# Kernel optimization log

Hardware: AMD Instinct MI355X
Metric: run time of the kernel (lower is better)

Reference implementation:

```python
import jax, jax.numpy as jnp
import numpy as np

_EPS = 1e-8

def setup_inputs() -> dict:
    key = jax.random.key(0)
    k1, k2, k3, k4 = jax.random.split(key, 4)
    L, B, H, S = 12, 8, 12, 384
    M, NL, NH = 32, 3, 4
    attn = jax.random.uniform(k1, (L, B, H, S, S), dtype=jnp.float32)
    references = jax.random.uniform(k2, (M, S, S), dtype=jnp.float32)
    layer_idx = jax.random.randint(k3, (M, NL), 0, L)
    head_idx = jax.random.randint(k4, (M, NH), 0, H)
    return {"attn": attn, "references": references,
            "layer_idx": layer_idx, "head_idx": head_idx}

def reference(attn, references, layer_idx, head_idx):
    # attn: [L,B,H,S,S] stacked attention maps; references: [M,S,S]
    L, B, H, S, _ = attn.shape
    M, nl = layer_idx.shape
    nh = head_idx.shape[1]
    rows = jnp.arange(M)[:, None]
    # One-hot averaging matrices: patch mean over selected layers/heads.
    # .add handles repeated indices the same way the gather-then-mean does.
    Wl = jnp.zeros((M, L), attn.dtype).at[rows, layer_idx].add(1.0 / nl)
    Wh = jnp.zeros((M, H), attn.dtype).at[rows, head_idx].add(1.0 / nh)
    # patch_means[m,b,s,t] = mean over patch layers/heads of attn
    patch_means = jnp.einsum('ml,mh,lbhst->mbst', Wl, Wh, attn)  # [M,B,S,S]
    flat = patch_means.reshape(M, B, S * S)
    ref = references.reshape(M, 1, S * S)
    # torch .std is unbiased (ddof=1) over the batch axis
    std = jnp.maximum(jnp.std(flat, axis=1, ddof=1, keepdims=True), _EPS)
    z = (flat - ref) / std
    scores = jnp.mean(z * z, axis=-1)  # [M,B]
    return scores.T  # [B,M]
```

## Files before the change

kernel.cpp:

```cpp
#include <hip/hip_runtime.h>

#define L_DIM 12
#define B_DIM 8
#define H_DIM 12
#define S2    147456
#define M_DIM 32
#define NL 3
#define NH 4
#define HS2   (H_DIM * S2)

#define C      128
#define NCH    (S2 / C)
#define RED1   32
#define NRED1  (NCH / RED1)

#define PART_FLOATS (NCH * 256)
#define MID_FLOATS  (NRED1 * 256)
#define META_INTS   2048

__global__ __launch_bounds__(256) void pfe_setup(
    const int* __restrict__ lidx, const int* __restrict__ hidx, int* __restrict__ mi)
{
    __shared__ unsigned char s_cl[M_DIM][16];
    __shared__ unsigned char s_ch[M_DIM][16];
    __shared__ int s_used[144];
    __shared__ int s_slot[144];
    const int t = threadIdx.x;
    for (int i = t; i < 1176; i += 256) mi[168 + i] = 0;
    if (t < M_DIM) {
        for (int l = 0; l < L_DIM; ++l) s_cl[t][l] = 0;
        for (int h = 0; h < H_DIM; ++h) s_ch[t][h] = 0;
        for (int i = 0; i < NL; ++i) s_cl[t][lidx[t * NL + i]]++;
        for (int j = 0; j < NH; ++j) s_ch[t][hidx[t * NH + j]]++;
    }
    __syncthreads();
    if (t < 144) {
        const int l = t / H_DIM, h = t % H_DIM;
        int u = 0;
        for (int m = 0; m < M_DIM; ++m) u |= (s_cl[m][l] && s_ch[m][h]) ? 1 : 0;
        s_used[t] = u;
    }
    __syncthreads();
    if (t == 0) {
        int np = 0, lastb = 0;
        for (int k = 0; k < 144; ++k) {
            if (s_used[k]) {
                s_slot[k] = np;
                lastb = ((k / H_DIM) * (B_DIM * H_DIM) + (k % H_DIM)) * S2;
                mi[8 + np] = lastb;
                ++np;
            } else s_slot[k] = -1;
        }
        for (int p = np; p < 160; ++p) mi[8 + p] = lastb;
        mi[0] = np;
    }
    __syncthreads();
    if (t < 144) {
        const int sl = s_slot[t];
        if (sl >= 0) {
            const int l = t / H_DIM, h = t % H_DIM;
            int wd[8] = {0, 0, 0, 0, 0, 0, 0, 0};
#pragma unroll
            for (int g = 0; g < 8; ++g) {
                int w = 0;
#pragma unroll
                for (int j = 0; j < 4; ++j) {
                    const int m = g * 4 + j;
                    w |= ((int)s_cl[m][l] * (int)s_ch[m][h]) << (8 * j);
                }
                wd[g] = w;
            }
            int* wp = mi + 168 + sl * 8;
#pragma unroll
            for (int g = 0; g < 8; ++g) wp[g] = wd[g];
        }
    }
}

__global__ __launch_bounds__(256) void pfe_gather(
    const float* __restrict__ attn, const float* __restrict__ refs,
    const int* __restrict__ mi, float* __restrict__ part)
{
    __shared__ int s_pbase[160];
    __shared__ int s_ww[1176];
    __shared__ float s_x[8 * B_DIM * C];

    const int t = threadIdx.x;
    for (int i = t; i < 160; i += 256) s_pbase[i] = mi[8 + i];
    for (int i = t; i < 1176; i += 256) s_ww[i] = mi[168 + i];
    const int np4 = (mi[0] + 3) & ~3;
    __syncthreads();

    const int b = t >> 5, q = t & 31;
    const unsigned off0 = (unsigned)blockIdx.x * C;
    const unsigned fixoff = (unsigned)b * (unsigned)HS2 + off0 + (unsigned)q * 4u;

    float4 acc[M_DIM];
#pragma unroll
    for (int m = 0; m < M_DIM; ++m) acc[m] = make_float4(0.f, 0.f, 0.f, 0.f);

#define LD(P) (*reinterpret_cast<const float4*>(attn + (unsigned)s_pbase[P] + fixoff))

#define PROC_WORD(SW, G, V)                                             \
    if (SW) {                                                           \
        const float f0 = (float)((SW) & 255);                           \
        const float f1 = (float)(((SW) >> 8) & 255);                    \
        const float f2 = (float)(((SW) >> 16) & 255);                   \
        const float f3 = (float)(((SW) >> 24) & 255);                   \
        acc[4*(G)+0].x = fmaf(f0, (V).x, acc[4*(G)+0].x);               \
        acc[4*(G)+0].y = fmaf(f0, (V).y, acc[4*(G)+0].y);               \
        acc[4*(G)+0].z = fmaf(f0, (V).z, acc[4*(G)+0].z);               \
        acc[4*(G)+0].w = fmaf(f0, (V).w, acc[4*(G)+0].w);               \
        acc[4*(G)+1].x = fmaf(f1, (V).x, acc[4*(G)+1].x);               \
        acc[4*(G)+1].y = fmaf(f1, (V).y, acc[4*(G)+1].y);               \
        acc[4*(G)+1].z = fmaf(f1, (V).z, acc[4*(G)+1].z);               \
        acc[4*(G)+1].w = fmaf(f1, (V).w, acc[4*(G)+1].w);               \
        acc[4*(G)+2].x = fmaf(f2, (V).x, acc[4*(G)+2].x);               \
        acc[4*(G)+2].y = fmaf(f2, (V).y, acc[4*(G)+2].y);               \
        acc[4*(G)+2].z = fmaf(f2, (V).z, acc[4*(G)+2].z);               \
        acc[4*(G)+2].w = fmaf(f2, (V).w, acc[4*(G)+2].w);               \
        acc[4*(G)+3].x = fmaf(f3, (V).x, acc[4*(G)+3].x);               \
        acc[4*(G)+3].y = fmaf(f3, (V).y, acc[4*(G)+3].y);               \
        acc[4*(G)+3].z = fmaf(f3, (V).z, acc[4*(G)+3].z);               \
        acc[4*(G)+3].w = fmaf(f3, (V).w, acc[4*(G)+3].w);               \
    }

#define PROC_PLANE(P, V)                                                \
    {                                                                   \
        const int4 wa = *reinterpret_cast<const int4*>(s_ww + (P) * 8); \
        const int4 wb = *reinterpret_cast<const int4*>(s_ww + (P) * 8 + 4); \
        const int w0 = __builtin_amdgcn_readfirstlane(wa.x);            \
        const int w1 = __builtin_amdgcn_readfirstlane(wa.y);            \
        const int w2 = __builtin_amdgcn_readfirstlane(wa.z);            \
        const int w3 = __builtin_amdgcn_readfirstlane(wa.w);            \
        const int w4 = __builtin_amdgcn_readfirstlane(wb.x);            \
        const int w5 = __builtin_amdgcn_readfirstlane(wb.y);            \
        const int w6 = __builtin_amdgcn_readfirstlane(wb.z);            \
        const int w7 = __builtin_amdgcn_readfirstlane(wb.w);            \
        PROC_WORD(w0, 0, V) PROC_WORD(w1, 1, V)                         \
        PROC_WORD(w2, 2, V) PROC_WORD(w3, 3, V)                         \
        PROC_WORD(w4, 4, V) PROC_WORD(w5, 5, V)                         \
        PROC_WORD(w6, 6, V) PROC_WORD(w7, 7, V)                         \
    }

    float4 n0 = LD(0), n1 = LD(1), n2 = LD(2), n3 = LD(3);
    for (int p = 0; p < np4; p += 4) {
        const float4 c0 = n0, c1 = n1, c2 = n2, c3 = n3;
        n0 = LD(p + 4); n1 = LD(p + 5); n2 = LD(p + 6); n3 = LD(p + 7);
        PROC_PLANE(p + 0, c0)
        PROC_PLANE(p + 1, c1)
        PROC_PLANE(p + 2, c2)
        PROC_PLANE(p + 3, c3)
    }
#undef PROC_PLANE
#undef PROC_WORD
#undef LD

    const float c12 = 1.0f / 12.0f;
    const int mm = t >> 5;

    for (int sl = 0; sl < 4; ++sl) {
        __syncthreads();
#pragma unroll
        for (int k = 0; k < 8; ++k) {
            const float4 a = acc[sl * 8 + k];
            float4 p;
            p.x = a.x * c12; p.y = a.y * c12; p.z = a.z * c12; p.w = a.w * c12;
            *reinterpret_cast<float4*>(&s_x[(k * B_DIM + b) * C + q * 4]) = p;
        }
        __syncthreads();

        const int m = sl * 8 + mm;
        float4 x[B_DIM];
#pragma unroll
        for (int bb = 0; bb < B_DIM; ++bb)
            x[bb] = *reinterpret_cast<const float4*>(&s_x[(mm * B_DIM + bb) * C + q * 4]);
        float4 mu = make_float4(0.f, 0.f, 0.f, 0.f);
#pragma unroll
        for (int bb = 0; bb < B_DIM; ++bb) {
            mu.x += x[bb].x; mu.y += x[bb].y; mu.z += x[bb].z; mu.w += x[bb].w;
        }
        mu.x *= 0.125f; mu.y *= 0.125f; mu.z *= 0.125f; mu.w *= 0.125f;
        float4 ss = make_float4(0.f, 0.f, 0.f, 0.f);
#pragma unroll
        for (int bb = 0; bb < B_DIM; ++bb) {
            const float dx = x[bb].x - mu.x, dy = x[bb].y - mu.y,
                        dz = x[bb].z - mu.z, dw = x[bb].w - mu.w;
            ss.x = fmaf(dx, dx, ss.x); ss.y = fmaf(dy, dy, ss.y);
            ss.z = fmaf(dz, dz, ss.z); ss.w = fmaf(dw, dw, ss.w);
        }
        const float c7 = 1.0f / 7.0f;
        float4 inv;
        inv.x = 1.0f / fmaxf(sqrtf(ss.x * c7), 1e-8f);
        inv.y = 1.0f / fmaxf(sqrtf(ss.y * c7), 1e-8f);
        inv.z = 1.0f / fmaxf(sqrtf(ss.z * c7), 1e-8f);
        inv.w = 1.0f / fmaxf(sqrtf(ss.w * c7), 1e-8f);
        const float4 rv = *reinterpret_cast<const float4*>(
            refs + (size_t)m * S2 + off0 + (unsigned)q * 4u);

        float zs[B_DIM];
#pragma unroll
        for (int bb = 0; bb < B_DIM; ++bb) {
            const float zx = (x[bb].x - rv.x) * inv.x;
            const float zy = (x[bb].y - rv.y) * inv.y;
            const float zz = (x[bb].z - rv.z) * inv.z;
            const float zw = (x[bb].w - rv.w) * inv.w;
            zs[bb] = fmaf(zx, zx, fmaf(zy, zy, fmaf(zz, zz, zw * zw)));
        }
#pragma unroll
        for (int bb = 0; bb < B_DIM; ++bb) {
            float v = zs[bb];
            v += __shfl_xor(v, 1);
            v += __shfl_xor(v, 2);
            v += __shfl_xor(v, 4);
            v += __shfl_xor(v, 8);
            v += __shfl_xor(v, 16);
            zs[bb] = v;
        }
        if (q == 0) {
            float* pp = part + blockIdx.x * 256 + m * B_DIM;
            *reinterpret_cast<float4*>(pp) =
                make_float4(zs[0], zs[1], zs[2], zs[3]);
            *reinterpret_cast<float4*>(pp + 4) =
                make_float4(zs[4], zs[5], zs[6], zs[7]);
        }
    }
}

__global__ __launch_bounds__(256) void pfe_red1(
    const float* __restrict__ part, float* __restrict__ mid)
{
    const int t = threadIdx.x;
    const int c0 = blockIdx.x * RED1;
    float s = 0.f;
#pragma unroll
    for (int i = 0; i < RED1; ++i) s += part[(c0 + i) * 256 + t];
    mid[blockIdx.x * 256 + t] = s;
}

__global__ __launch_bounds__(256) void pfe_red2(
    const float* __restrict__ mid, float* __restrict__ out)
{
    const int t = threadIdx.x;
    float s = 0.f;
#pragma unroll
    for (int i = 0; i < NRED1; ++i) s += mid[i * 256 + t];
    out[(t & 7) * M_DIM + (t >> 3)] = s * (1.0f / (float)S2);
}

__global__ void pfe_zero(float* __restrict__ out) {
    if (threadIdx.x < M_DIM * B_DIM) out[threadIdx.x] = 0.f;
}

#define FCH 512
#define FNCH (S2 / FCH)
__global__ __launch_bounds__(128) void pfe_fallback(
    const float* __restrict__ attn, const float* __restrict__ refs,
    const int* __restrict__ lidx, const int* __restrict__ hidx,
    float* __restrict__ out)
{
    const int p = blockIdx.x;
    const int m = p & (M_DIM - 1);
    const int chunk = p >> 5;
    const int tid = threadIdx.x;
    const unsigned st = (unsigned)chunk * FCH + (unsigned)tid * 4;

    __shared__ int   s_mk[NL * NH];
    __shared__ float s_mw[NL * NH];
    __shared__ int   s_nm;
    __shared__ float s_red[2 * B_DIM];

    if (tid == 0) {
        int keys[NL * NH];
        for (int i = 0; i < NL; ++i) {
            const int l = lidx[m * NL + i];
            for (int j = 0; j < NH; ++j) keys[i * NH + j] = l * 16 + hidx[m * NH + j];
        }
        for (int i = 1; i < NL * NH; ++i) {
            const int k = keys[i]; int j = i - 1;
            for (; j >= 0 && keys[j] > k; --j) keys[j + 1] = keys[j];
            keys[j + 1] = k;
        }
        int nm = 0;
        for (int i = 0; i < NL * NH; ++i) {
            if (nm > 0 && s_mk[nm - 1] == keys[i]) s_mw[nm - 1] += 1.0f;
            else { s_mk[nm] = keys[i]; s_mw[nm] = 1.0f; ++nm; }
        }
        s_nm = nm;
    }
    __syncthreads();

    const float4 r = *reinterpret_cast<const float4*>(refs + (unsigned)m * (unsigned)S2 + st);
    float4 acc[B_DIM];
    for (int bb = 0; bb < B_DIM; ++bb) acc[bb] = make_float4(0.f, 0.f, 0.f, 0.f);
    const int nm = s_nm;
    for (int e = 0; e < nm; ++e) {
        const int k = s_mk[e]; const float w = s_mw[e];
        const int l = k >> 4, h = k & 15;
        const unsigned base = (unsigned)(l * (B_DIM * H_DIM) + h) * (unsigned)S2 + st;
        for (int bb = 0; bb < B_DIM; ++bb) {
            const float4 v = *reinterpret_cast<const float4*>(
                attn + base + (unsigned)bb * (unsigned)HS2);
            acc[bb].x = fmaf(w, v.x, acc[bb].x); acc[bb].y = fmaf(w, v.y, acc[bb].y);
            acc[bb].z = fmaf(w, v.z, acc[bb].z); acc[bb].w = fmaf(w, v.w, acc[bb].w);
        }
    }
    const float c12 = 1.0f / 12.0f;
    float4 pmv[B_DIM];
    for (int bb = 0; bb < B_DIM; ++bb) {
        pmv[bb].x = acc[bb].x * c12; pmv[bb].y = acc[bb].y * c12;
        pmv[bb].z = acc[bb].z * c12; pmv[bb].w = acc[bb].w * c12;
    }
    float4 mu = make_float4(0.f, 0.f, 0.f, 0.f);
    for (int bb = 0; bb < B_DIM; ++bb) {
        mu.x += pmv[bb].x; mu.y += pmv[bb].y; mu.z += pmv[bb].z; mu.w += pmv[bb].w;
    }
    mu.x *= 0.125f; mu.y *= 0.125f; mu.z *= 0.125f; mu.w *= 0.125f;
    float4 ss = make_float4(0.f, 0.f, 0.f, 0.f);
    for (int bb = 0; bb < B_DIM; ++bb) {
        const float dx = pmv[bb].x - mu.x, dy = pmv[bb].y - mu.y,
                    dz = pmv[bb].z - mu.z, dw = pmv[bb].w - mu.w;
        ss.x += dx * dx; ss.y += dy * dy; ss.z += dz * dz; ss.w += dw * dw;
    }
    const float c7 = 1.0f / 7.0f;
    float4 inv;
    inv.x = 1.0f / fmaxf(sqrtf(ss.x * c7), 1e-8f);
    inv.y = 1.0f / fmaxf(sqrtf(ss.y * c7), 1e-8f);
    inv.z = 1.0f / fmaxf(sqrtf(ss.z * c7), 1e-8f);
    inv.w = 1.0f / fmaxf(sqrtf(ss.w * c7), 1e-8f);
    float s[B_DIM];
    for (int bb = 0; bb < B_DIM; ++bb) {
        const float zx = (pmv[bb].x - r.x) * inv.x;
        const float zy = (pmv[bb].y - r.y) * inv.y;
        const float zz = (pmv[bb].z - r.z) * inv.z;
        const float zw = (pmv[bb].w - r.w) * inv.w;
        s[bb] = zx * zx + zy * zy + zz * zz + zw * zw;
    }
    for (int bb = 0; bb < B_DIM; ++bb) {
        float v = s[bb];
        for (int off = 32; off > 0; off >>= 1) v += __shfl_down(v, off);
        s[bb] = v;
    }
    const int lane = tid & 63, wave = tid >> 6;
    if (lane == 0) for (int bb = 0; bb < B_DIM; ++bb) s_red[wave * B_DIM + bb] = s[bb];
    __syncthreads();
    if (tid < B_DIM) {
        const float tot = (s_red[tid] + s_red[B_DIM + tid]) * (1.0f / (float)S2);
        atomicAdd(&out[tid * M_DIM + m], tot);
    }
}

extern "C" void kernel_launch(void* const* d_in, const int* in_sizes, int n_in,
                              void* d_out, int out_size, void* d_ws, size_t ws_size,
                              hipStream_t stream) {
    const float* attn = (const float*)d_in[0];
    const float* refs = (const float*)d_in[1];
    const int*   lidx = (const int*)d_in[2];
    const int*   hidx = (const int*)d_in[3];
    float* out = (float*)d_out;

    const size_t ws_needed =
        (size_t)(PART_FLOATS + MID_FLOATS + META_INTS) * sizeof(float);

    if (ws_size >= ws_needed) {
        float* part = (float*)d_ws;
        float* mid  = part + PART_FLOATS;
        int*   mi   = (int*)(mid + MID_FLOATS);
        pfe_setup<<<1, 256, 0, stream>>>(lidx, hidx, mi);
        pfe_gather<<<NCH, 256, 0, stream>>>(attn, refs, mi, part);
        pfe_red1<<<NRED1, 256, 0, stream>>>(part, mid);
        pfe_red2<<<1, 256, 0, stream>>>(mid, out);
    } else {
        pfe_zero<<<1, 256, 0, stream>>>(out);
        pfe_fallback<<<FNCH * M_DIM, 128, 0, stream>>>(attn, refs, lidx, hidx, out);
    }
}
```

Measured before the change: 164.3 us.

## Halve per-thread gather width to float2 with 512-thread blocks for occupancy

The gather kernel now uses 512 threads per block, each handling two columns instead of four. This halves the accumulator registers (32 float2 instead of 32 float4) so more waves can be resident to hide memory latency. It also deepens the load prefetch from 4 to 8 planes and prefetches the reference values one slice ahead. In exchange each load is narrower (8-byte instead of 16-byte), and the cross-lane reduction needs an extra shuffle step because the batch groups are now full 64-lane wavefronts.

```diff
diff --git a/kernel.cpp b/kernel.cpp
--- a/kernel.cpp
+++ b/kernel.cpp
@@ -77,7 +77,7 @@
     }
 }
 
-__global__ __launch_bounds__(256) void pfe_gather(
+__global__ __launch_bounds__(512, 4) void pfe_gather(
     const float* __restrict__ attn, const float* __restrict__ refs,
     const int* __restrict__ mi, float* __restrict__ part)
 {
@@ -86,20 +86,20 @@
     __shared__ float s_x[8 * B_DIM * C];
 
     const int t = threadIdx.x;
-    for (int i = t; i < 160; i += 256) s_pbase[i] = mi[8 + i];
-    for (int i = t; i < 1176; i += 256) s_ww[i] = mi[168 + i];
-    const int np4 = (mi[0] + 3) & ~3;
-    __syncthreads();
-
-    const int b = t >> 5, q = t & 31;
+    for (int i = t; i < 160; i += 512) s_pbase[i] = mi[8 + i];
+    for (int i = t; i < 1176; i += 512) s_ww[i] = mi[168 + i];
+    const int np8 = (mi[0] + 7) & ~7;
+    __syncthreads();
+
+    const int b = t >> 6, q = t & 63;
     const unsigned off0 = (unsigned)blockIdx.x * C;
-    const unsigned fixoff = (unsigned)b * (unsigned)HS2 + off0 + (unsigned)q * 4u;
-
-    float4 acc[M_DIM];
-#pragma unroll
-    for (int m = 0; m < M_DIM; ++m) acc[m] = make_float4(0.f, 0.f, 0.f, 0.f);
-
-#define LD(P) (*reinterpret_cast<const float4*>(attn + (unsigned)s_pbase[P] + fixoff))
+    const unsigned fixoff = (unsigned)b * (unsigned)HS2 + off0 + (unsigned)q * 2u;
+
+    float2 acc[M_DIM];
+#pragma unroll
+    for (int m = 0; m < M_DIM; ++m) acc[m] = make_float2(0.f, 0.f);
+
+#define LD(P) (*reinterpret_cast<const float2*>(attn + (unsigned)s_pbase[P] + fixoff))
 
 #define PROC_WORD(SW, G, V)                                             \
     if (SW) {                                                           \
@@ -109,20 +109,12 @@
         const float f3 = (float)(((SW) >> 24) & 255);                   \
         acc[4*(G)+0].x = fmaf(f0, (V).x, acc[4*(G)+0].x);               \
         acc[4*(G)+0].y = fmaf(f0, (V).y, acc[4*(G)+0].y);               \
-        acc[4*(G)+0].z = fmaf(f0, (V).z, acc[4*(G)+0].z);               \
-        acc[4*(G)+0].w = fmaf(f0, (V).w, acc[4*(G)+0].w);               \
         acc[4*(G)+1].x = fmaf(f1, (V).x, acc[4*(G)+1].x);               \
         acc[4*(G)+1].y = fmaf(f1, (V).y, acc[4*(G)+1].y);               \
-        acc[4*(G)+1].z = fmaf(f1, (V).z, acc[4*(G)+1].z);               \
-        acc[4*(G)+1].w = fmaf(f1, (V).w, acc[4*(G)+1].w);               \
         acc[4*(G)+2].x = fmaf(f2, (V).x, acc[4*(G)+2].x);               \
         acc[4*(G)+2].y = fmaf(f2, (V).y, acc[4*(G)+2].y);               \
-        acc[4*(G)+2].z = fmaf(f2, (V).z, acc[4*(G)+2].z);               \
-        acc[4*(G)+2].w = fmaf(f2, (V).w, acc[4*(G)+2].w);               \
         acc[4*(G)+3].x = fmaf(f3, (V).x, acc[4*(G)+3].x);               \
         acc[4*(G)+3].y = fmaf(f3, (V).y, acc[4*(G)+3].y);               \
-        acc[4*(G)+3].z = fmaf(f3, (V).z, acc[4*(G)+3].z);               \
-        acc[4*(G)+3].w = fmaf(f3, (V).w, acc[4*(G)+3].w);               \
     }
 
 #define PROC_PLANE(P, V)                                                \
@@ -143,69 +135,75 @@
         PROC_WORD(w6, 6, V) PROC_WORD(w7, 7, V)                         \
     }
 
-    float4 n0 = LD(0), n1 = LD(1), n2 = LD(2), n3 = LD(3);
-    for (int p = 0; p < np4; p += 4) {
-        const float4 c0 = n0, c1 = n1, c2 = n2, c3 = n3;
-        n0 = LD(p + 4); n1 = LD(p + 5); n2 = LD(p + 6); n3 = LD(p + 7);
+    float2 n0 = LD(0), n1 = LD(1), n2 = LD(2), n3 = LD(3),
+           n4 = LD(4), n5 = LD(5), n6 = LD(6), n7 = LD(7);
+    for (int p = 0; p < np8; p += 8) {
+        const float2 c0 = n0, c1 = n1, c2 = n2, c3 = n3,
+                     c4 = n4, c5 = n5, c6 = n6, c7 = n7;
+        n0 = LD(p + 8);  n1 = LD(p + 9);  n2 = LD(p + 10); n3 = LD(p + 11);
+        n4 = LD(p + 12); n5 = LD(p + 13); n6 = LD(p + 14); n7 = LD(p + 15);
         PROC_PLANE(p + 0, c0)
         PROC_PLANE(p + 1, c1)
         PROC_PLANE(p + 2, c2)
         PROC_PLANE(p + 3, c3)
+        PROC_PLANE(p + 4, c4)
+        PROC_PLANE(p + 5, c5)
+        PROC_PLANE(p + 6, c6)
+        PROC_PLANE(p + 7, c7)
     }
 #undef PROC_PLANE
 #undef PROC_WORD
 #undef LD
 
     const float c12 = 1.0f / 12.0f;
-    const int mm = t >> 5;
-
+    const int mm = t >> 6;
+
+    float2 rv_next = *reinterpret_cast<const float2*>(
+        refs + (size_t)mm * S2 + off0 + (unsigned)q * 2u);
+
+#pragma unroll
     for (int sl = 0; sl < 4; ++sl) {
         __syncthreads();
 #pragma unroll
         for (int k = 0; k < 8; ++k) {
-            const float4 a = acc[sl * 8 + k];
-            float4 p;
-            p.x = a.x * c12; p.y = a.y * c12; p.z = a.z * c12; p.w = a.w * c12;
-            *reinterpret_cast<float4*>(&s_x[(k * B_DIM + b) * C + q * 4]) = p;
+            const float2 a = acc[sl * 8 + k];
+            float2 p;
+            p.x = a.x * c12; p.y = a.y * c12;
+            *reinterpret_cast<float2*>(&s_x[(k * B_DIM + b) * C + q * 2]) = p;
         }
         __syncthreads();
 
         const int m = sl * 8 + mm;
-        float4 x[B_DIM];
+        const float2 rv = rv_next;
+        if (sl < 3) {
+            rv_next = *reinterpret_cast<const float2*>(
+                refs + (size_t)(m + 8) * S2 + off0 + (unsigned)q * 2u);
+        }
+        float2 x[B_DIM];
 #pragma unroll
         for (int bb = 0; bb < B_DIM; ++bb)
-            x[bb] = *reinterpret_cast<const float4*>(&s_x[(mm * B_DIM + bb) * C + q * 4]);
-        float4 mu = make_float4(0.f, 0.f, 0.f, 0.f);
+            x[bb] = *reinterpret_cast<const float2*>(&s_x[(mm * B_DIM + bb) * C + q * 2]);
+        float2 mu = make_float2(0.f, 0.f);
+#pragma unroll
+        for (int bb = 0; bb < B_DIM; ++bb) { mu.x += x[bb].x; mu.y += x[bb].y; }
+        mu.x *= 0.125f; mu.y *= 0.125f;
+        float2 ss = make_float2(0.f, 0.f);
 #pragma unroll
         for (int bb = 0; bb < B_DIM; ++bb) {
-            mu.x += x[bb].x; mu.y += x[bb].y; mu.z += x[bb].z; mu.w += x[bb].w;
-        }
-        mu.x *= 0.125f; mu.y *= 0.125f; mu.z *= 0.125f; mu.w *= 0.125f;
-        float4 ss = make_float4(0.f, 0.f, 0.f, 0.f);
-#pragma unroll
-        for (int bb = 0; bb < B_DIM; ++bb) {
-            const float dx = x[bb].x - mu.x, dy = x[bb].y - mu.y,
-                        dz = x[bb].z - mu.z, dw = x[bb].w - mu.w;
+            const float dx = x[bb].x - mu.x, dy = x[bb].y - mu.y;
             ss.x = fmaf(dx, dx, ss.x); ss.y = fmaf(dy, dy, ss.y);
-            ss.z = fmaf(dz, dz, ss.z); ss.w = fmaf(dw, dw, ss.w);
         }
         const float c7 = 1.0f / 7.0f;
-        float4 inv;
+        float2 inv;
         inv.x = 1.0f / fmaxf(sqrtf(ss.x * c7), 1e-8f);
         inv.y = 1.0f / fmaxf(sqrtf(ss.y * c7), 1e-8f);
-        inv.z = 1.0f / fmaxf(sqrtf(ss.z * c7), 1e-8f);
-        inv.w = 1.0f / fmaxf(sqrtf(ss.w * c7), 1e-8f);
-        const float4 rv = *reinterpret_cast<const float4*>(
-            refs + (size_t)m * S2 + off0 + (unsigned)q * 4u);
 
         float zs[B_DIM];
 #pragma unroll
         for (int bb = 0; bb < B_DIM; ++bb) {
             const float zx = (x[bb].x - rv.x) * inv.x;
             const float zy = (x[bb].y - rv.y) * inv.y;
-            const float zz = (x[bb].z - rv.z) * inv.z;
-            const float zw = (x[bb].w - rv.w) * inv.w;
-            zs[bb] = fmaf(zx, zx, fmaf(zy, zy, fmaf(zz, zz, zw * zw)));
+            zs[bb] = fmaf(zx, zx, zy * zy);
         }
 #pragma unroll
         for (int bb = 0; bb < B_DIM; ++bb) {
@@ -215,6 +213,7 @@
             v += __shfl_xor(v, 4);
             v += __shfl_xor(v, 8);
             v += __shfl_xor(v, 16);
+            v += __shfl_xor(v, 32);
             zs[bb] = v;
         }
         if (q == 0) {
@@ -367,7 +366,7 @@
         float* mid  = part + PART_FLOATS;
         int*   mi   = (int*)(mid + MID_FLOATS);
         pfe_setup<<<1, 256, 0, stream>>>(lidx, hidx, mi);
-        pfe_gather<<<NCH, 256, 0, stream>>>(attn, refs, mi, part);
+        pfe_gather<<<NCH, 512, 0, stream>>>(attn, refs, mi, part);
         pfe_red1<<<NRED1, 256, 0, stream>>>(part, mid);
         pfe_red2<<<1, 256, 0, stream>>>(mid, out);
     } else {
```

Measured after the change: 165.3 us. Within noise of the previous version (+0.6%).
